# Kernel optimization log

Hardware: AMD Instinct MI355X
Metric: run time of the kernel (lower is better)

Reference implementation:

```python
import jax, jax.numpy as jnp
import numpy as np

NUM_HEADS = 32
HIDDEN = 4096
HEAD_DIM = HIDDEN // NUM_HEADS
BATCH = 1
SEQ = 2048


def setup_inputs() -> dict:
    key = jax.random.key(0)
    ks = jax.random.split(key, 8)
    hidden_states = jax.random.normal(ks[0], (BATCH, SEQ, HIDDEN), dtype=jnp.float32)
    residual = jax.random.normal(ks[1], (BATCH, SEQ, HIDDEN), dtype=jnp.float32)
    # BLOOM alibi: [batch*heads, 1, kv_len], broadcast over q_length in baddbmm
    alibi = jax.random.normal(ks[2], (BATCH * NUM_HEADS, 1, SEQ), dtype=jnp.float32) * 0.1
    # causal boolean mask: True = masked (filled with -inf before softmax)
    attention_mask = ~jnp.tril(jnp.ones((SEQ, SEQ), dtype=bool))[None, None, :, :]
    scale = 0.02
    Wqkv = jax.random.normal(ks[3], (3 * HIDDEN, HIDDEN), dtype=jnp.float32) * scale
    bqkv = jax.random.normal(ks[4], (3 * HIDDEN,), dtype=jnp.float32) * scale
    Wd = jax.random.normal(ks[5], (HIDDEN, HIDDEN), dtype=jnp.float32) * scale
    bd = jax.random.normal(ks[6], (HIDDEN,), dtype=jnp.float32) * scale
    return {"hidden_states": hidden_states, "residual": residual, "alibi": alibi,
            "attention_mask": attention_mask, "Wqkv": Wqkv, "bqkv": bqkv,
            "Wd": Wd, "bd": bd}


def reference(hidden_states, residual, alibi, attention_mask, Wqkv, bqkv, Wd, bd):
    B, S, H = hidden_states.shape
    nh, hd = NUM_HEADS, HEAD_DIM
    inv_norm = 1.0 / np.sqrt(hd).astype(np.float32)

    # fused QKV projection, BLOOM interleaved layout [B, S, nh, 3, hd]
    fused = hidden_states @ Wqkv.T + bqkv           # [B, S, 3H]
    fused = fused.reshape(B, S, nh, 3, hd)
    q = jnp.transpose(fused[..., 0, :], (0, 2, 1, 3))  # [B, nh, S, hd]
    k = jnp.transpose(fused[..., 1, :], (0, 2, 1, 3))  # [B, nh, S, hd]
    v = jnp.transpose(fused[..., 2, :], (0, 2, 1, 3))  # [B, nh, S, hd]

    # baddbmm: alibi + inv_norm * Q @ K^T
    alibi_b = alibi.reshape(B, nh, 1, S)                # broadcast over q_length
    scores = alibi_b + inv_norm * jnp.einsum('bhqd,bhkd->bhqk', q, k)
    scores = jnp.where(attention_mask, jnp.finfo(scores.dtype).min, scores)
    probs = jax.nn.softmax(scores, axis=-1)             # [B, nh, S, S]

    ctx = jnp.einsum('bhqk,bhkd->bhqd', probs, v)       # [B, nh, S, hd]
    ctx = jnp.transpose(ctx, (0, 2, 1, 3)).reshape(B, S, H)
    out = ctx @ Wd.T + bd
    return residual + out
```

## Files before the change

### kernel.cpp

```cpp
#include <hip/hip_runtime.h>


#define SEQL 2048
#define HIDN 4096
#define NHEAD 32
#define HDIM 128
#define H3 12288

typedef __bf16 bf16x8 __attribute__((ext_vector_type(8)));
typedef float f32x4 __attribute__((ext_vector_type(4)));
typedef unsigned short u16x8 __attribute__((ext_vector_type(8)));

__device__ __forceinline__ unsigned short f2bf(float f) {
  union { float f; unsigned u; } v; v.f = f;
  return (unsigned short)((v.u + 0x7FFFu + ((v.u >> 16) & 1u)) >> 16);
}

__device__ __forceinline__ void gload_lds16(const void* g, void* l) {
  __builtin_amdgcn_global_load_lds(
      (const __attribute__((address_space(1))) void*)g,
      (__attribute__((address_space(3))) void*)l, 16, 0, 0);
}

#define BAR() __builtin_amdgcn_s_barrier()
#define SCHED0() __builtin_amdgcn_sched_barrier(0x7)
#define VM(n) asm volatile("s_waitcnt vmcnt(" #n ")" ::: "memory")

__global__ __launch_bounds__(256) void cvt_f32_bf16(
    const float* __restrict__ in, unsigned short* __restrict__ out, long long n) {
  long long i = ((long long)blockIdx.x * blockDim.x + threadIdx.x) * 8;
  long long stride = (long long)gridDim.x * blockDim.x * 8;
  for (; i < n; i += stride) {
    float4 a = *(const float4*)(in + i);
    float4 b = *(const float4*)(in + i + 4);
    u16x8 o;
    o[0] = f2bf(a.x); o[1] = f2bf(a.y); o[2] = f2bf(a.z); o[3] = f2bf(a.w);
    o[4] = f2bf(b.x); o[5] = f2bf(b.y); o[6] = f2bf(b.z); o[7] = f2bf(b.w);
    *(u16x8*)(out + i) = o;
  }
}

__global__ __launch_bounds__(512, 2) void gemm256_qkv(
    const unsigned short* __restrict__ A, const unsigned short* __restrict__ B,
    const float* __restrict__ bias,
    unsigned short* __restrict__ q_bf, unsigned short* __restrict__ k_bf,
    unsigned short* __restrict__ v_t) {
  __shared__ unsigned short Ab[2][2][8192];
  __shared__ unsigned short Bb[2][2][8192];

  const int tid = threadIdx.x;
  const int l = tid & 63;
  const int w = tid >> 6;
  const int K = HIDN;

  const int b = blockIdx.x;
  const int lin = (b & 7) * 48 + (b >> 3);
  const int tm0 = (lin & 7) * 256;
  const int tn0 = (lin >> 3) * 256;

  const int lr = l >> 3;
  const int lc = (l & 7) ^ lr;
  const int wm = w >> 2;
  const int wn = w & 3;
  const int bhalf = wn >> 1;
  const int brow0 = (wn & 1) * 64;

  f32x4 acc[2][2][4][2] = {};
  bf16x8 A0s[4][2], A1s[4][2], B0s[2][2], B1s[2][2];

  auto stA = [&](int tt, int h) {
#pragma unroll
    for (int i = 0; i < 2; ++i) {
      const int c = w * 2 + i;
      gload_lds16(&A[(long long)(tm0 + h * 128 + c * 8 + lr) * K + tt * 64 + lc * 8],
                  (char*)&Ab[tt & 1][h][0] + c * 1024);
    }
  };
  auto stB = [&](int tt, int h) {
#pragma unroll
    for (int i = 0; i < 2; ++i) {
      const int c = w * 2 + i;
      gload_lds16(&B[(long long)(tn0 + h * 128 + c * 8 + lr) * K + tt * 64 + lc * 8],
                  (char*)&Bb[tt & 1][h][0] + c * 1024);
    }
  };
  auto rdA = [&](bf16x8 (&dst)[4][2], int bufi, int mh) {
#pragma unroll
    for (int mi = 0; mi < 4; ++mi) {
      const int r = mh * 64 + mi * 16 + (l & 15);
#pragma unroll
      for (int kk = 0; kk < 2; ++kk)
        dst[mi][kk] = *(const bf16x8*)((const char*)&Ab[bufi][wm][0] +
            r * 128 + ((kk * 64 + (l >> 4) * 16) ^ ((r & 7) << 4)));
    }
  };
  auto rdB = [&](bf16x8 (&dst)[2][2], int bufi, int nh) {
#pragma unroll
    for (int ni = 0; ni < 2; ++ni) {
      const int r = brow0 + nh * 32 + ni * 16 + (l & 15);
#pragma unroll
      for (int kk = 0; kk < 2; ++kk)
        dst[ni][kk] = *(const bf16x8*)((const char*)&Bb[bufi][bhalf][0] +
            r * 128 + ((kk * 64 + (l >> 4) * 16) ^ ((r & 7) << 4)));
    }
  };

#define MFMA16(As_, Bs_, mh_, nh_)                                            \
  __builtin_amdgcn_s_setprio(1);                                              \
  _Pragma("unroll") for (int kk = 0; kk < 2; ++kk)                            \
    _Pragma("unroll") for (int mi = 0; mi < 4; ++mi)                          \
      _Pragma("unroll") for (int ni = 0; ni < 2; ++ni)                        \
        acc[mh_][nh_][mi][ni] = __builtin_amdgcn_mfma_f32_16x16x32_bf16(      \
            As_[mi][kk], Bs_[ni][kk], acc[mh_][nh_][mi][ni], 0, 0, 0);        \
  __builtin_amdgcn_s_setprio(0);

  stA(0, 0); stB(0, 0); stB(0, 1); stA(0, 1);
  VM(2);
  BAR();
  SCHED0();
  rdA(A0s, 0, 0);
  rdB(B0s, 0, 0);
  SCHED0();

  const int NT = K / 64;
  for (int t = 0; t < NT; ++t) {
    const int bf = t & 1;
    const bool pf = (t + 1) < NT;
    if (pf) { stA(t + 1, 0); VM(4); } else { VM(2); }
    BAR(); SCHED0();
    MFMA16(A0s, B0s, 0, 0);
    rdB(B1s, bf, 1);
    SCHED0(); BAR();
    if (pf) { stB(t + 1, 0); VM(4); } else { VM(0); }
    BAR(); SCHED0();
    MFMA16(A0s, B1s, 0, 1);
    rdA(A1s, bf, 1);
    SCHED0(); BAR();
    if (pf) { stB(t + 1, 1); }
    BAR(); SCHED0();
    MFMA16(A1s, B0s, 1, 0);
    SCHED0(); BAR();
    if (pf) { stA(t + 1, 1); VM(4); }
    BAR(); SCHED0();
    MFMA16(A1s, B1s, 1, 1);
    if (pf) {
      rdA(A0s, bf ^ 1, 0);
      rdB(B0s, bf ^ 1, 0);
    }
    SCHED0(); BAR();
  }

#pragma unroll
  for (int mh = 0; mh < 2; ++mh)
#pragma unroll
    for (int nh = 0; nh < 2; ++nh)
#pragma unroll
      for (int mi = 0; mi < 4; ++mi)
#pragma unroll
        for (int ni = 0; ni < 2; ++ni) {
          const int col = tn0 + wn * 64 + nh * 32 + ni * 16 + (l & 15);
          const float bv = bias[col];
          const int head = col / 384;
          const int rem = col - head * 384;
          const int which = rem >> 7;
          const int d = rem & 127;
#pragma unroll
          for (int r = 0; r < 4; ++r) {
            const int row = tm0 + wm * 128 + mh * 64 + mi * 16 + (l >> 4) * 4 + r;
            const unsigned short bv16 = f2bf(acc[mh][nh][mi][ni][r] + bv);
            if (which == 0)
              q_bf[(long long)(head * SEQL + row) * HDIM + d] = bv16;
            else if (which == 1)
              k_bf[(long long)(head * SEQL + row) * HDIM + d] = bv16;
            else
              v_t[(long long)(head * HDIM + d) * SEQL + row] = bv16;
          }
        }
}

__global__ __launch_bounds__(256) void gemm_nt_res(
    const unsigned short* __restrict__ A, const unsigned short* __restrict__ B,
    int M, int N, int K,
    const float* __restrict__ bias, const float* __restrict__ residual,
    float* __restrict__ outf) {
  __shared__ unsigned short As[128 * 64];
  __shared__ unsigned short Bs[128 * 64];

  const int tid = threadIdx.x;
  const int l = tid & 63;
  const int w = tid >> 6;
  const int wr = (w >> 1) * 64;
  const int wc = (w & 1) * 64;
  const int tm0 = blockIdx.x * 128;
  const int tn0 = blockIdx.y * 128;

  const int lr = l >> 3;
  const int lc = (l & 7) ^ lr;

  f32x4 acc[4][4] = {};

  for (int kt = 0; kt < K; kt += 64) {
    __syncthreads();
#pragma unroll
    for (int i = 0; i < 4; ++i) {
      const int row = w * 32 + i * 8 + lr;
      gload_lds16(&A[(long long)(tm0 + row) * K + kt + lc * 8],
                  (char*)As + (w * 4 + i) * 1024);
      gload_lds16(&B[(long long)(tn0 + row) * K + kt + lc * 8],
                  (char*)Bs + (w * 4 + i) * 1024);
    }
    __syncthreads();
#pragma unroll
    for (int kk = 0; kk < 2; ++kk) {
      const int colb = kk * 64 + (l >> 4) * 16;
      bf16x8 af[4], bfr[4];
#pragma unroll
      for (int m = 0; m < 4; ++m) {
        int row = wr + m * 16 + (l & 15);
        af[m] = *(const bf16x8*)((char*)As + row * 128 + (colb ^ ((row & 7) << 4)));
      }
#pragma unroll
      for (int n = 0; n < 4; ++n) {
        int row = wc + n * 16 + (l & 15);
        bfr[n] = *(const bf16x8*)((char*)Bs + row * 128 + (colb ^ ((row & 7) << 4)));
      }
#pragma unroll
      for (int m = 0; m < 4; ++m)
#pragma unroll
        for (int n = 0; n < 4; ++n)
          acc[m][n] = __builtin_amdgcn_mfma_f32_16x16x32_bf16(af[m], bfr[n], acc[m][n], 0, 0, 0);
    }
  }

#pragma unroll
  for (int m = 0; m < 4; ++m)
#pragma unroll
    for (int n = 0; n < 4; ++n) {
      const int col = tn0 + wc + n * 16 + (l & 15);
      const float bv = bias[col];
#pragma unroll
      for (int r = 0; r < 4; ++r) {
        const int rowg = tm0 + wr + m * 16 + (l >> 4) * 4 + r;
        const long long idx = (long long)rowg * N + col;
        outf[idx] = acc[m][n][r] + bv + residual[idx];
      }
    }
}

__global__ __launch_bounds__(256) void attn_fwd(
    const unsigned short* __restrict__ q_bf, const unsigned short* __restrict__ k_bf,
    const unsigned short* __restrict__ v_t, const float* __restrict__ alibi,
    unsigned short* __restrict__ ctx_bf) {
  __shared__ unsigned short Ks[64 * 128];
  __shared__ unsigned short Vs[128 * 64];
  __shared__ unsigned short Ps[4][16 * 64];
  __shared__ float Al[SEQL];

  const int tid = threadIdx.x;
  const int l = tid & 63;
  const int w = tid >> 6;
  const int h = blockIdx.x;
  const int qt = blockIdx.y * 64;
  const int qw = qt + w * 16;

  for (int i = tid; i < SEQL; i += 256) Al[i] = alibi[h * SEQL + i];

  bf16x8 qf[4];
  {
    const unsigned short* qp =
        &q_bf[(long long)(h * SEQL + qw + (l & 15)) * HDIM + (l >> 4) * 8];
#pragma unroll
    for (int kk = 0; kk < 4; ++kk) qf[kk] = *(const bf16x8*)(qp + kk * 32);
  }

  f32x4 oacc[8] = {};
  float mrun[4] = {-__builtin_inff(), -__builtin_inff(), -__builtin_inff(), -__builtin_inff()};
  float lrun[4] = {0.f, 0.f, 0.f, 0.f};
  const float inv_norm = 0.08838834764831845f;

  const int kR = l >> 4, kC = l & 15;
  const int vR = l >> 3, vC = (l & 7) ^ vR;

  const int ntiles = blockIdx.y + 1;
  for (int t = 0; t < ntiles; ++t) {
    const int kv0 = t * 64;
    __syncthreads();
#pragma unroll
    for (int i = 0; i < 4; ++i) {
      const int krow = w * 16 + i * 4 + kR;
      const int ksrc = kC ^ ((i & 1) * 4 + kR);
      gload_lds16(&k_bf[(long long)(h * SEQL + kv0 + krow) * HDIM + ksrc * 8],
                  (char*)Ks + (w * 4 + i) * 1024);
      const int vrow = w * 32 + i * 8 + vR;
      gload_lds16(&v_t[(long long)(h * HDIM + vrow) * SEQL + kv0 + vC * 8],
                  (char*)Vs + (w * 4 + i) * 1024);
    }
    __syncthreads();

    f32x4 sacc[4] = {};
#pragma unroll
    for (int kk = 0; kk < 4; ++kk) {
      const int colb = kk * 64 + (l >> 4) * 16;
#pragma unroll
      for (int n = 0; n < 4; ++n) {
        int row = n * 16 + (l & 15);
        bf16x8 kf = *(const bf16x8*)((char*)Ks + row * 256 + (colb ^ ((row & 7) << 4)));
        sacc[n] = __builtin_amdgcn_mfma_f32_16x16x32_bf16(qf[kk], kf, sacc[n], 0, 0, 0);
      }
    }

    float sc[4][4];
#pragma unroll
    for (int n = 0; n < 4; ++n) {
      const int kv = kv0 + n * 16 + (l & 15);
      const float al = Al[kv];
#pragma unroll
      for (int r = 0; r < 4; ++r) {
        const int qrow = qw + (l >> 4) * 4 + r;
        float v = al + inv_norm * sacc[n][r];
        sc[n][r] = (kv > qrow) ? -__builtin_inff() : v;
      }
    }

#pragma unroll
    for (int r = 0; r < 4; ++r) {
      float m0 = fmaxf(fmaxf(sc[0][r], sc[1][r]), fmaxf(sc[2][r], sc[3][r]));
      m0 = fmaxf(m0, __shfl_xor(m0, 1, 64));
      m0 = fmaxf(m0, __shfl_xor(m0, 2, 64));
      m0 = fmaxf(m0, __shfl_xor(m0, 4, 64));
      m0 = fmaxf(m0, __shfl_xor(m0, 8, 64));
      const float mnew = fmaxf(mrun[r], m0);
      float p0 = 0.f;
#pragma unroll
      for (int n = 0; n < 4; ++n) {
        const float pv = __expf(sc[n][r] - mnew);
        sc[n][r] = pv;
        p0 += pv;
      }
      p0 += __shfl_xor(p0, 1, 64);
      p0 += __shfl_xor(p0, 2, 64);
      p0 += __shfl_xor(p0, 4, 64);
      p0 += __shfl_xor(p0, 8, 64);
      const float scale = __expf(mrun[r] - mnew);
      mrun[r] = mnew;
      lrun[r] = lrun[r] * scale + p0;
#pragma unroll
      for (int n2 = 0; n2 < 8; ++n2) oacc[n2][r] *= scale;
    }

#pragma unroll
    for (int n = 0; n < 4; ++n)
#pragma unroll
      for (int r = 0; r < 4; ++r) {
        const int row = (l >> 4) * 4 + r;
        const int colp = n * 16 + (l & 15);
        *(unsigned short*)((char*)Ps[w] + row * 128 + ((colp * 2) ^ ((row & 7) << 4))) =
            f2bf(sc[n][r]);
      }
    __threadfence_block();
    bf16x8 pf[2];
#pragma unroll
    for (int kk2 = 0; kk2 < 2; ++kk2) {
      const int row = l & 15;
      const int colb = kk2 * 64 + (l >> 4) * 16;
      pf[kk2] = *(const bf16x8*)((char*)Ps[w] + row * 128 + (colb ^ ((row & 7) << 4)));
    }

#pragma unroll
    for (int n2 = 0; n2 < 8; ++n2) {
#pragma unroll
      for (int kk2 = 0; kk2 < 2; ++kk2) {
        const int row = n2 * 16 + (l & 15);
        const int colb = kk2 * 64 + (l >> 4) * 16;
        bf16x8 vf = *(const bf16x8*)((char*)Vs + row * 128 + (colb ^ ((row & 7) << 4)));
        oacc[n2] = __builtin_amdgcn_mfma_f32_16x16x32_bf16(pf[kk2], vf, oacc[n2], 0, 0, 0);
      }
    }
  }

#pragma unroll
  for (int n2 = 0; n2 < 8; ++n2)
#pragma unroll
    for (int r = 0; r < 4; ++r) {
      const int qrow = qw + (l >> 4) * 4 + r;
      const int col = h * HDIM + n2 * 16 + (l & 15);
      ctx_bf[(long long)qrow * HIDN + col] = f2bf(oacc[n2][r] / lrun[r]);
    }
}

extern "C" void kernel_launch(void* const* d_in, const int* in_sizes, int n_in,
                              void* d_out, int out_size, void* d_ws, size_t ws_size,
                              hipStream_t stream) {
  const float* hidden = (const float*)d_in[0];
  const float* residual = (const float*)d_in[1];
  const float* alibi = (const float*)d_in[2];
  const float* Wqkv = (const float*)d_in[4];
  const float* bqkv = (const float*)d_in[5];
  const float* Wd = (const float*)d_in[6];
  const float* bd = (const float*)d_in[7];
  float* out = (float*)d_out;

  char* ws = (char*)d_ws;
  const size_t MB16 = 16777216;
  unsigned short* q_bf = (unsigned short*)(ws);
  unsigned short* k_bf = (unsigned short*)(ws + MB16);
  unsigned short* v_t = (unsigned short*)(ws + 2 * MB16);
  unsigned short* hid_bf = (unsigned short*)(ws + 3 * MB16);
  unsigned short* wqkv_bf = (unsigned short*)(ws + 4 * MB16);
  unsigned short* wd_bf = (unsigned short*)(ws + 4 * MB16);
  unsigned short* ctx_bf = (unsigned short*)(ws + 4 * MB16 + 33554432);

  cvt_f32_bf16<<<4096, 256, 0, stream>>>(hidden, hid_bf, (long long)SEQL * HIDN);
  cvt_f32_bf16<<<24576, 256, 0, stream>>>(Wqkv, wqkv_bf, (long long)H3 * HIDN);

  gemm256_qkv<<<384, 512, 0, stream>>>(hid_bf, wqkv_bf, bqkv, q_bf, k_bf, v_t);

  cvt_f32_bf16<<<8192, 256, 0, stream>>>(Wd, wd_bf, (long long)HIDN * HIDN);

  attn_fwd<<<dim3(NHEAD, SEQL / 64), 256, 0, stream>>>(q_bf, k_bf, v_t, alibi, ctx_bf);

  gemm_nt_res<<<dim3(SEQL / 128, HIDN / 128), 256, 0, stream>>>(
      ctx_bf, wd_bf, SEQL, HIDN, HIDN, bd, residual, out);
}
```

Baseline: 514.0 us.

## Reschedule QKV GEMM pipeline, remap warp tiles, and reorder attention/GEMM block dispatch

The QKV GEMM main loop is unrolled by two k-tiles with explicit lgkmcnt waits and full sched barriers. Its warp-to-subtile mapping changes so each warp reads both A and B halves, and more global-to-LDS prefetches are kept in flight. The output GEMM gets a 1D grid with an XCD-aware block remap, and attention blocks are dispatched longest-causal-tile-first with heads interleaved across XCDs. The aim is better MFMA/load overlap, load balance and L2 locality, at the cost of a fragile hand-tuned schedule with a risk of races in the LDS double buffer.

```diff
diff --git a/kernel.cpp b/kernel.cpp
--- a/kernel.cpp
+++ b/kernel.cpp
@@ -23,8 +23,9 @@
 }
 
 #define BAR() __builtin_amdgcn_s_barrier()
-#define SCHED0() __builtin_amdgcn_sched_barrier(0x7)
-#define VM(n) asm volatile("s_waitcnt vmcnt(" #n ")" ::: "memory")
+#define SB0() __builtin_amdgcn_sched_barrier(0)
+#define VMW(n) asm volatile("s_waitcnt vmcnt(" #n ")" ::: "memory")
+#define LGKM(n) asm volatile("s_waitcnt lgkmcnt(" #n ")" ::: "memory")
 
 __global__ __launch_bounds__(256) void cvt_f32_bf16(
     const float* __restrict__ in, unsigned short* __restrict__ out, long long n) {
@@ -60,10 +61,8 @@
 
   const int lr = l >> 3;
   const int lc = (l & 7) ^ lr;
-  const int wm = w >> 2;
-  const int wn = w & 3;
-  const int bhalf = wn >> 1;
-  const int brow0 = (wn & 1) * 64;
+  const int wr2 = w >> 2;
+  const int wc2 = w & 3;
 
   f32x4 acc[2][2][4][2] = {};
   bf16x8 A0s[4][2], A1s[4][2], B0s[2][2], B1s[2][2];
@@ -84,23 +83,23 @@
                   (char*)&Bb[tt & 1][h][0] + c * 1024);
     }
   };
-  auto rdA = [&](bf16x8 (&dst)[4][2], int bufi, int mh) {
+  auto rdA = [&](bf16x8 (&dst)[4][2], int bufi, int h) {
 #pragma unroll
     for (int mi = 0; mi < 4; ++mi) {
-      const int r = mh * 64 + mi * 16 + (l & 15);
+      const int r = wr2 * 64 + mi * 16 + (l & 15);
 #pragma unroll
       for (int kk = 0; kk < 2; ++kk)
-        dst[mi][kk] = *(const bf16x8*)((const char*)&Ab[bufi][wm][0] +
+        dst[mi][kk] = *(const bf16x8*)((const char*)&Ab[bufi][h][0] +
             r * 128 + ((kk * 64 + (l >> 4) * 16) ^ ((r & 7) << 4)));
     }
   };
-  auto rdB = [&](bf16x8 (&dst)[2][2], int bufi, int nh) {
+  auto rdB = [&](bf16x8 (&dst)[2][2], int bufi, int h) {
 #pragma unroll
     for (int ni = 0; ni < 2; ++ni) {
-      const int r = brow0 + nh * 32 + ni * 16 + (l & 15);
+      const int r = wc2 * 32 + ni * 16 + (l & 15);
 #pragma unroll
       for (int kk = 0; kk < 2; ++kk)
-        dst[ni][kk] = *(const bf16x8*)((const char*)&Bb[bufi][bhalf][0] +
+        dst[ni][kk] = *(const bf16x8*)((const char*)&Bb[bufi][h][0] +
             r * 128 + ((kk * 64 + (l >> 4) * 16) ^ ((r & 7) << 4)));
     }
   };
@@ -115,39 +114,62 @@
   __builtin_amdgcn_s_setprio(0);
 
   stA(0, 0); stB(0, 0); stB(0, 1); stA(0, 1);
-  VM(2);
+  stA(1, 0); stB(1, 1);
+  VMW(4);
   BAR();
-  SCHED0();
-  rdA(A0s, 0, 0);
-  rdB(B0s, 0, 0);
-  SCHED0();
 
   const int NT = K / 64;
-  for (int t = 0; t < NT; ++t) {
-    const int bf = t & 1;
-    const bool pf = (t + 1) < NT;
-    if (pf) { stA(t + 1, 0); VM(4); } else { VM(2); }
-    BAR(); SCHED0();
+  const int NITER = NT / 2;
+  for (int j = 0; j < NITER; ++j) {
+    const int bT = 2 * j + 1, c = 2 * j + 2, dT = 2 * j + 3;
+    const bool g = (j + 1) < NITER;
+    rdA(A0s, 0, 0);
+    rdB(B0s, 0, 0);
+    stB(bT, 0);
+    LGKM(8);
+    SB0(); BAR();
+    LGKM(0); SB0();
     MFMA16(A0s, B0s, 0, 0);
-    rdB(B1s, bf, 1);
-    SCHED0(); BAR();
-    if (pf) { stB(t + 1, 0); VM(4); } else { VM(0); }
-    BAR(); SCHED0();
+    SB0(); BAR();
+    rdB(B1s, 0, 1);
+    stA(bT, 1);
+    SB0(); BAR();
+    LGKM(0); SB0();
     MFMA16(A0s, B1s, 0, 1);
-    rdA(A1s, bf, 1);
-    SCHED0(); BAR();
-    if (pf) { stB(t + 1, 1); }
-    BAR(); SCHED0();
+    SB0(); BAR();
+    rdA(A1s, 0, 1);
+    if (g) stA(c, 0);
+    SB0(); BAR();
+    LGKM(0); SB0();
+    MFMA16(A1s, B1s, 1, 1);
+    SB0(); BAR();
+    if (g) { stB(c, 1); VMW(4); } else { VMW(0); }
+    SB0(); BAR();
     MFMA16(A1s, B0s, 1, 0);
-    SCHED0(); BAR();
-    if (pf) { stA(t + 1, 1); VM(4); }
-    BAR(); SCHED0();
+    SB0(); BAR();
+    rdA(A0s, 1, 0);
+    rdB(B0s, 1, 0);
+    if (g) { stA(c, 1); stB(c, 0); }
+    LGKM(8);
+    SB0(); BAR();
+    LGKM(0); SB0();
+    MFMA16(A0s, B0s, 0, 0);
+    SB0(); BAR();
+    rdB(B1s, 1, 1);
+    SB0(); BAR();
+    LGKM(0); SB0();
+    MFMA16(A0s, B1s, 0, 1);
+    SB0(); BAR();
+    rdA(A1s, 1, 1);
+    if (g) stA(dT, 0);
+    SB0(); BAR();
+    LGKM(0); SB0();
     MFMA16(A1s, B1s, 1, 1);
-    if (pf) {
-      rdA(A0s, bf ^ 1, 0);
-      rdB(B0s, bf ^ 1, 0);
-    }
-    SCHED0(); BAR();
+    SB0(); BAR();
+    if (g) { stB(dT, 1); VMW(4); }
+    SB0(); BAR();
+    MFMA16(A1s, B0s, 1, 0);
+    SB0(); BAR();
   }
 
 #pragma unroll
@@ -158,7 +180,7 @@
       for (int mi = 0; mi < 4; ++mi)
 #pragma unroll
         for (int ni = 0; ni < 2; ++ni) {
-          const int col = tn0 + wn * 64 + nh * 32 + ni * 16 + (l & 15);
+          const int col = tn0 + nh * 128 + wc2 * 32 + ni * 16 + (l & 15);
           const float bv = bias[col];
           const int head = col / 384;
           const int rem = col - head * 384;
@@ -166,7 +188,7 @@
           const int d = rem & 127;
 #pragma unroll
           for (int r = 0; r < 4; ++r) {
-            const int row = tm0 + wm * 128 + mh * 64 + mi * 16 + (l >> 4) * 4 + r;
+            const int row = tm0 + mh * 128 + wr2 * 64 + mi * 16 + (l >> 4) * 4 + r;
             const unsigned short bv16 = f2bf(acc[mh][nh][mi][ni][r] + bv);
             if (which == 0)
               q_bf[(long long)(head * SEQL + row) * HDIM + d] = bv16;
@@ -191,8 +213,11 @@
   const int w = tid >> 6;
   const int wr = (w >> 1) * 64;
   const int wc = (w & 1) * 64;
-  const int tm0 = blockIdx.x * 128;
-  const int tn0 = blockIdx.y * 128;
+
+  const int nb = gridDim.x;
+  const int lin = (blockIdx.x & 7) * (nb >> 3) + (blockIdx.x >> 3);
+  const int tm0 = (lin & 15) * 128;
+  const int tn0 = (lin >> 4) * 128;
 
   const int lr = l >> 3;
   const int lc = (l & 7) ^ lr;
@@ -259,9 +284,12 @@
   const int tid = threadIdx.x;
   const int l = tid & 63;
   const int w = tid >> 6;
-  const int h = blockIdx.x;
-  const int qt = blockIdx.y * 64;
-  const int qw = qt + w * 16;
+
+  const int b = blockIdx.x;
+  const int i_ = b >> 3;
+  const int h = (b & 7) * 4 + (i_ & 3);
+  const int qtile = 31 - (i_ >> 2);
+  const int qw = qtile * 64 + w * 16;
 
   for (int i = tid; i < SEQL; i += 256) Al[i] = alibi[h * SEQL + i];
 
@@ -281,7 +309,7 @@
   const int kR = l >> 4, kC = l & 15;
   const int vR = l >> 3, vC = (l & 7) ^ vR;
 
-  const int ntiles = blockIdx.y + 1;
+  const int ntiles = qtile + 1;
   for (int t = 0; t < ntiles; ++t) {
     const int kv0 = t * 64;
     __syncthreads();
@@ -417,8 +445,8 @@
 
   cvt_f32_bf16<<<8192, 256, 0, stream>>>(Wd, wd_bf, (long long)HIDN * HIDN);
 
-  attn_fwd<<<dim3(NHEAD, SEQL / 64), 256, 0, stream>>>(q_bf, k_bf, v_t, alibi, ctx_bf);
-
-  gemm_nt_res<<<dim3(SEQL / 128, HIDN / 128), 256, 0, stream>>>(
+  attn_fwd<<<NHEAD * (SEQL / 64), 256, 0, stream>>>(q_bf, k_bf, v_t, alibi, ctx_bf);
+
+  gemm_nt_res<<<(SEQL / 128) * (HIDN / 128), 256, 0, stream>>>(
       ctx_bf, wd_bf, SEQL, HIDN, HIDN, bd, residual, out);
 }
```

New measurement: 491.2 us. -4.4%, faster.
